# Kernel tuning notes

Hardware: AMD Instinct MI355X
Metric: run time of the kernel (lower is better)

## Reference

```python
import jax, jax.numpy as jnp
import numpy as np

B, S, D = 2, 2048, 1024
H, DH = 16, 64
C = 64          # chunk_size (sliding window)
WF = 4          # widening factor
FMIN = jnp.finfo(jnp.float32).min


def _ln(x, scale, offset, eps=1e-5):
    mu = jnp.mean(x, axis=-1, keepdims=True)
    var = jnp.var(x, axis=-1, keepdims=True)
    return (x - mu) * jax.lax.rsqrt(var + eps) * scale + offset


def setup_inputs() -> dict:
    key = jax.random.key(0)
    ks = jax.random.split(key, 12)
    std = 0.02
    inp = {
        'x': jax.random.normal(ks[0], (B, S, D), dtype=jnp.float32),
        'causal_mask': jnp.tril(jnp.ones((S, S), dtype=bool))[None, None],  # (1,1,S,S)
        'pos': jax.random.normal(ks[1], (C, D), dtype=jnp.float32),          # pos_0..pos_{C-1}
        'rpe': std * jax.random.normal(ks[2], (H, C), dtype=jnp.float32),
        'Wq': std * jax.random.normal(ks[3], (D, H * DH), dtype=jnp.float32),
        'Wk': std * jax.random.normal(ks[4], (D, H * DH), dtype=jnp.float32),
        'Wv': std * jax.random.normal(ks[5], (D, H * DH), dtype=jnp.float32),
        'Wo': std * jax.random.normal(ks[6], (H * DH, D), dtype=jnp.float32),
        'ln1_scale': jnp.ones((D,), jnp.float32),
        'ln1_offset': jnp.zeros((D,), jnp.float32),
        'W1': std * jax.random.normal(ks[7], (D, WF * D), dtype=jnp.float32),
        'b1': jnp.zeros((WF * D,), jnp.float32),
        'W2': std * jax.random.normal(ks[8], (WF * D, D), dtype=jnp.float32),
        'b2': jnp.zeros((D,), jnp.float32),
        'ln2_scale': jnp.ones((D,), jnp.float32),
        'ln2_offset': jnp.zeros((D,), jnp.float32),
    }
    return inp


def _sliding_window_mask(rpe, seq_len):
    # mask[h,t,T] = rpe[h, t-T] if 0 <= t-T < C (lower diagonals), else -inf
    d = jnp.arange(seq_len)[:, None] - jnp.arange(seq_len)[None, :]  # (S,S)
    valid = (d >= 0) & (d < C)
    dc = jnp.clip(d, 0, C - 1)
    val = jnp.where(valid[None], rpe[:, dc], 0.0)  # (H,S,S)
    return jnp.where(val != 0, val, FMIN)


def reference(x, causal_mask, pos, rpe, Wq, Wk, Wv, Wo, ln1_scale, ln1_offset,
              W1, b1, W2, b2, ln2_scale, ln2_offset):
    seq_len = x.shape[1]
    # front/rear positional vectors: pos_i added at positions i, i+C, i+2C, ...
    h = x + pos[jnp.arange(seq_len) % C]  # (B,S,D)

    q = (h @ Wq).reshape(B, seq_len, H, DH)
    k = (h @ Wk).reshape(B, seq_len, H, DH)
    v = (h @ Wv).reshape(B, seq_len, H, DH)

    attn = jnp.einsum('bthd,bThd->bhtT', q, k) * (1.0 / jnp.sqrt(DH))
    attn = attn + _sliding_window_mask(rpe, seq_len)[None]  # learned diag bias
    attn = jnp.where(causal_mask, attn, FMIN)
    attn = jax.nn.softmax(attn, axis=-1)

    out = jnp.einsum('bhtT,bThd->bthd', attn, v).reshape(B, seq_len, H * DH)
    out = out @ Wo

    # dropout_prob = 0 -> identity
    attention = _ln(h + out, ln1_scale, ln1_offset)
    ff = jax.nn.relu(attention @ W1 + b1) @ W2 + b2
    return _ln(ff + attention, ln2_scale, ln2_offset)
```

## Files before the change

### kernel.cpp

```cpp
#include <hip/hip_runtime.h>
#include <hip/hip_bf16.h>

#define DEVI static __device__ __forceinline__

typedef __attribute__((ext_vector_type(4))) float f32x4;
typedef __attribute__((ext_vector_type(8))) short bf16x8;
typedef __attribute__((ext_vector_type(4))) short s16x4;

constexpr int TB  = 2;
constexpr int TS  = 2048;
constexpr int TD  = 1024;
constexpr int TH  = 16;
constexpr int TDH = 64;
constexpr int TC  = 64;
constexpr int TFF = 4096;
constexpr int TM  = TB * TS;

DEVI float bf2f(short s) {
  return __builtin_bit_cast(float, (unsigned)((unsigned short)s) << 16);
}
DEVI short f2bf(float f) {
  return __builtin_bit_cast(short, __float2bfloat16(f));
}

#define GLD16(gp, lp)                                              \
  __builtin_amdgcn_global_load_lds(                                \
      (const __attribute__((address_space(1))) void*)(gp),         \
      (__attribute__((address_space(3))) void*)(lp), 16, 0, 0)

#define WAITVM(N) asm volatile("s_waitcnt vmcnt(" #N ")" ::: "memory")

__global__ __launch_bounds__(256) void k_transpose_bf16(
    const float* __restrict__ W, __hip_bfloat16* __restrict__ WT, int K, int N) {
  __shared__ float tile[32][33];
  int n0 = blockIdx.x * 32, k0 = blockIdx.y * 32;
  int tx = threadIdx.x & 31, ty = threadIdx.x >> 5;
  for (int i = 0; i < 32; i += 8)
    tile[ty + i][tx] = W[(size_t)(k0 + ty + i) * N + n0 + tx];
  __syncthreads();
  for (int i = 0; i < 32; i += 8)
    WT[(size_t)(n0 + ty + i) * K + k0 + tx] = __float2bfloat16(tile[tx][ty + i]);
}

__global__ __launch_bounds__(256) void k_addpos(
    const float* __restrict__ x, const float* __restrict__ pos,
    __hip_bfloat16* __restrict__ hb, int total4) {
  int i = blockIdx.x * 256 + threadIdx.x;
  if (i >= total4) return;
  int e = i * 4;
  int d = e & (TD - 1);
  int t = (e / TD) & (TS - 1);
  f32x4 xv = *(const f32x4*)(x + e);
  f32x4 pv = *(const f32x4*)(pos + (size_t)(t & (TC - 1)) * TD + d);
  s16x4 hb4;
  for (int j = 0; j < 4; j++) hb4[j] = f2bf(xv[j] + pv[j]);
  *(s16x4*)((short*)hb + e) = hb4;
}

template <int EPI>
__global__ __launch_bounds__(256, 3) void k_gemm(
    const __hip_bfloat16* __restrict__ A, const __hip_bfloat16* __restrict__ BT,
    void* __restrict__ Cout, const float* __restrict__ bias,
    int M, int N, int K, int lda, int ldb) {
  constexpr int BM = 128, BN = 128, BK = 32;
  __shared__ __align__(16) __hip_bfloat16 As[3][BM * BK];
  __shared__ __align__(16) __hip_bfloat16 Bs[3][BN * BK];
  int tid = threadIdx.x;
  int lane = tid & 63, wave = tid >> 6;
  int wm = wave >> 1, wn = wave & 1;
  int fr = lane & 15, fg = lane >> 4;
  int m0 = blockIdx.x * BM, n0 = blockIdx.y * BN;
  size_t koff = (size_t)blockIdx.z * K;
  const __hip_bfloat16* Ab = A + koff;
  const __hip_bfloat16* Bb = BT + koff;

  auto stage = [&](int s, int k0) {
#pragma unroll
    for (int i = 0; i < 2; i++) {
      int c = (wave * 2 + i) * 64 + lane;
      int row = c >> 2, seg = (c & 3) ^ ((row >> 1) & 3);
      GLD16(Ab + (size_t)(m0 + row) * lda + k0 + seg * 8,
            (char*)&As[s][0] + (wave * 2 + i) * 1024);
      GLD16(Bb + (size_t)(n0 + row) * ldb + k0 + seg * 8,
            (char*)&Bs[s][0] + (wave * 2 + i) * 1024);
    }
  };

  f32x4 acc[4][4] = {};
  const int nt = K / BK;
  stage(0, 0);
  stage(1, BK);
  int cur = 0;
  for (int t = 0; t < nt; t++) {
    if (t + 1 < nt) { WAITVM(4); } else { WAITVM(0); }
    __builtin_amdgcn_s_barrier();
    asm volatile("" ::: "memory");
    bf16x8 af[4], bfv[4];
#pragma unroll
    for (int m = 0; m < 4; m++) {
      int row = wm * 64 + m * 16 + fr;
      af[m] = *(const bf16x8*)((const char*)&As[cur][0] + row * 64 +
                               ((fg ^ ((row >> 1) & 3)) * 16));
    }
#pragma unroll
    for (int n = 0; n < 4; n++) {
      int row = wn * 64 + n * 16 + fr;
      bfv[n] = *(const bf16x8*)((const char*)&Bs[cur][0] + row * 64 +
                                ((fg ^ ((row >> 1) & 3)) * 16));
    }
    if (t + 2 < nt) {
      int nb = cur + 2; if (nb >= 3) nb -= 3;
      stage(nb, (t + 2) * BK);
    }
    __builtin_amdgcn_s_setprio(1);
#pragma unroll
    for (int m = 0; m < 4; m++)
#pragma unroll
      for (int n = 0; n < 4; n++)
        acc[m][n] = __builtin_amdgcn_mfma_f32_16x16x32_bf16(af[m], bfv[n],
                                                            acc[m][n], 0, 0, 0);
    __builtin_amdgcn_s_setprio(0);
    cur++; if (cur == 3) cur = 0;
  }

  float* Cf = (float*)Cout + (size_t)blockIdx.z * M * N;
#pragma unroll
  for (int m = 0; m < 4; m++)
#pragma unroll
    for (int n = 0; n < 4; n++) {
      int col = n0 + wn * 64 + n * 16 + fr;
#pragma unroll
      for (int j = 0; j < 4; j++) {
        int row = m0 + wm * 64 + m * 16 + fg * 4 + j;
        float v = acc[m][n][j];
        if (EPI == 1) { v += bias[col]; v = fmaxf(v, 0.f); }
        if (EPI == 2)
          Cf[(size_t)row * N + col] = v;
        else
          ((__hip_bfloat16*)Cout)[(size_t)row * N + col] = __float2bfloat16(v);
      }
    }
}

__global__ __launch_bounds__(256) void k_vtrans(
    const __hip_bfloat16* __restrict__ qkv, __hip_bfloat16* __restrict__ vT) {
  __shared__ short tile[64][68];
  int bh = blockIdx.x;
  int tb = blockIdx.y;
  int b = bh >> 4, h = bh & 15;
  int tid = threadIdx.x;
#pragma unroll
  for (int i = 0; i < 2; i++) {
    int c = i * 256 + tid;
    int trow = c >> 3, seg = c & 7;
    bf16x8 v = *(const bf16x8*)((const short*)qkv +
        (size_t)(b * TS + tb * 64 + trow) * 3072 + 2048 + h * TDH + seg * 8);
    s16x4 lo = {v[0], v[1], v[2], v[3]}, hi = {v[4], v[5], v[6], v[7]};
    *(s16x4*)&tile[trow][seg * 8] = lo;
    *(s16x4*)&tile[trow][seg * 8 + 4] = hi;
  }
  __syncthreads();
#pragma unroll
  for (int i2 = 0; i2 < 2; i2++) {
    int c = i2 * 256 + tid;
    int d = c >> 3, ts = c & 7;
    bf16x8 o;
#pragma unroll
    for (int j = 0; j < 8; j++) o[j] = tile[ts * 8 + j][d];
    *(bf16x8*)((short*)vT + (size_t)bh * TDH * TS + (size_t)d * TS +
               tb * 64 + ts * 8) = o;
  }
}

__global__ __launch_bounds__(256) void k_attn(
    const __hip_bfloat16* __restrict__ qkv, const __hip_bfloat16* __restrict__ vT,
    const float* __restrict__ rpe, __hip_bfloat16* __restrict__ out) {
  __shared__ __align__(16) short K_lds[128 * 64];
  __shared__ __align__(16) short VT_lds[64 * 128];
  __shared__ __align__(16) short P_lds[4][16 * 136];
  __shared__ float rpe_lds[TC];
  int tid = threadIdx.x, lane = tid & 63, wave = tid >> 6;
  int fr = lane & 15, g = lane >> 4;
  int blk = blockIdx.x;
  int qt = blk & 31, bh = blk >> 5;
  int h = bh & 15, b = bh >> 4;
  int t0 = qt * 64;
  const short* qg = (const short*)qkv;

  if (tid < TC) rpe_lds[tid] = rpe[h * TC + tid];

#pragma unroll
  for (int i = 0; i < 4; i++) {
    int cb = i * 256 + wave * 64;
    int c = cb + lane;
    int row = c >> 3, slot = c & 7;
    int seg = slot ^ (row & 7);
    int kr = t0 - 64 + row; if (kr < 0) kr = 0;
    GLD16(qg + ((size_t)(b * TS + kr) * 3072 + 1024 + h * TDH + seg * 8),
          (char*)K_lds + cb * 16);
  }
  const short* vg = (const short*)vT + (size_t)bh * TDH * TS;
#pragma unroll
  for (int i = 0; i < 4; i++) {
    int cb = i * 256 + wave * 64;
    int c = cb + lane;
    int row = c >> 4, slot = c & 15;
    int seg = slot ^ (row & 15);
    int tc = t0 - 64 + seg * 8; if (tc < 0) tc = 0;
    GLD16(vg + (size_t)row * TS + tc, (char*)VT_lds + cb * 16);
  }

  int qrow = t0 + wave * 16 + fr;
  const short* qptr = qg + ((size_t)(b * TS + qrow) * 3072 + h * TDH + g * 8);
  bf16x8 qf0 = *(const bf16x8*)qptr;
  bf16x8 qf1 = *(const bf16x8*)(qptr + 32);

  __syncthreads();

  f32x4 S[8] = {};
#pragma unroll
  for (int kk = 0; kk < 2; kk++) {
    bf16x8 a = kk ? qf1 : qf0;
#pragma unroll
    for (int nt = 0; nt < 8; nt++) {
      int row = nt * 16 + fr;
      int slot = (kk * 4 + g) ^ (row & 7);
      bf16x8 bfrag = *(const bf16x8*)((const char*)K_lds + row * 128 + slot * 16);
      S[nt] = __builtin_amdgcn_mfma_f32_16x16x32_bf16(a, bfrag, S[nt], 0, 0, 0);
    }
  }

  int wq = wave * 16;
#pragma unroll
  for (int r = 0; r < 4; r++) {
    int ql = g * 4 + r;
    float sc[8];
    float m = -3.4028235e38f;
#pragma unroll
    for (int nt = 0; nt < 8; nt++) {
      int jj = nt * 16 + fr;
      int d = wq + ql + 64 - jj;
      bool valid = (d >= 0) && (d < TC) && (t0 - 64 + jj >= 0);
      float v = valid ? (S[nt][r] * 0.125f + rpe_lds[d & (TC - 1)])
                      : -3.4028235e38f;
      sc[nt] = v;
      m = fmaxf(m, v);
    }
#pragma unroll
    for (int o = 1; o < 16; o <<= 1) m = fmaxf(m, __shfl_xor(m, o));
    float p[8], sum = 0.f;
#pragma unroll
    for (int nt = 0; nt < 8; nt++) { p[nt] = __expf(sc[nt] - m); sum += p[nt]; }
#pragma unroll
    for (int o = 1; o < 16; o <<= 1) sum += __shfl_xor(sum, o);
    float rs = 1.0f / sum;
#pragma unroll
    for (int nt = 0; nt < 8; nt++)
      P_lds[wave][ql * 136 + nt * 16 + fr] = f2bf(p[nt] * rs);
  }

  f32x4 O[4] = {};
#pragma unroll
  for (int kk = 0; kk < 4; kk++) {
    bf16x8 pa = *(const bf16x8*)((const char*)&P_lds[wave][0] +
                                 fr * 272 + kk * 64 + g * 16);
#pragma unroll
    for (int dt = 0; dt < 4; dt++) {
      int row = dt * 16 + fr;
      int slot = (kk * 4 + g) ^ (row & 15);
      bf16x8 vb = *(const bf16x8*)((const char*)VT_lds + row * 256 + slot * 16);
      O[dt] = __builtin_amdgcn_mfma_f32_16x16x32_bf16(pa, vb, O[dt], 0, 0, 0);
    }
  }

  size_t ob = ((size_t)(b * TS + t0 + wq + g * 4)) * TD + h * TDH;
#pragma unroll
  for (int dt = 0; dt < 4; dt++)
#pragma unroll
    for (int r = 0; r < 4; r++)
      ((short*)out)[ob + (size_t)r * TD + dt * 16 + fr] = f2bf(O[dt][r]);
}

DEVI float block_sum(float v, float* red) {
  for (int o = 32; o; o >>= 1) v += __shfl_xor(v, o);
  int wave = threadIdx.x >> 6;
  if ((threadIdx.x & 63) == 0) red[wave] = v;
  __syncthreads();
  float r = red[0] + red[1] + red[2] + red[3];
  __syncthreads();
  return r;
}

__global__ __launch_bounds__(256) void k_ln1(
    const float* __restrict__ x, const float* __restrict__ pos,
    const float* __restrict__ P0, const float* __restrict__ P1,
    const float* __restrict__ scale, const float* __restrict__ offset,
    float* __restrict__ outf, __hip_bfloat16* __restrict__ outb) {
  __shared__ float red[4];
  int row = blockIdx.x, tid = threadIdx.x;
  int t = row & (TS - 1), pr = t & (TC - 1);
  size_t base = (size_t)row * TD + tid * 4;
  f32x4 xv = *(const f32x4*)(x + base);
  f32x4 pv = *(const f32x4*)(pos + (size_t)pr * TD + tid * 4);
  f32x4 a0 = *(const f32x4*)(P0 + base);
  f32x4 a1 = *(const f32x4*)(P1 + base);
  xv = xv + pv + a0 + a1;
  float s = xv[0] + xv[1] + xv[2] + xv[3];
  s = block_sum(s, red);
  float mu = s * (1.f / TD);
  float s2 = 0.f;
  for (int j = 0; j < 4; j++) { float dlt = xv[j] - mu; s2 += dlt * dlt; }
  s2 = block_sum(s2, red);
  float rs = rsqrtf(s2 * (1.f / TD) + 1e-5f);
  f32x4 sc = *(const f32x4*)(scale + tid * 4);
  f32x4 of = *(const f32x4*)(offset + tid * 4);
  f32x4 y;
  for (int j = 0; j < 4; j++) y[j] = (xv[j] - mu) * rs * sc[j] + of[j];
  *(f32x4*)(outf + base) = y;
  s16x4 pb;
  for (int j = 0; j < 4; j++) pb[j] = f2bf(y[j]);
  *(s16x4*)((short*)outb + base) = pb;
}

__global__ __launch_bounds__(256) void k_ln2(
    const float* __restrict__ P0, const float* __restrict__ P1,
    const float* __restrict__ R, const float* __restrict__ bias,
    const float* __restrict__ scale, const float* __restrict__ offset,
    float* __restrict__ outf) {
  __shared__ float red[4];
  int row = blockIdx.x, tid = threadIdx.x;
  size_t base = (size_t)row * TD + tid * 4;
  f32x4 a0 = *(const f32x4*)(P0 + base);
  f32x4 a1 = *(const f32x4*)(P1 + base);
  f32x4 rv = *(const f32x4*)(R + base);
  f32x4 bi = *(const f32x4*)(bias + tid * 4);
  f32x4 xv = a0 + a1 + rv + bi;
  float s = xv[0] + xv[1] + xv[2] + xv[3];
  s = block_sum(s, red);
  float mu = s * (1.f / TD);
  float s2 = 0.f;
  for (int j = 0; j < 4; j++) { float dlt = xv[j] - mu; s2 += dlt * dlt; }
  s2 = block_sum(s2, red);
  float rs = rsqrtf(s2 * (1.f / TD) + 1e-5f);
  f32x4 sc = *(const f32x4*)(scale + tid * 4);
  f32x4 of = *(const f32x4*)(offset + tid * 4);
  f32x4 y;
  for (int j = 0; j < 4; j++) y[j] = (xv[j] - mu) * rs * sc[j] + of[j];
  *(f32x4*)(outf + base) = y;
}

extern "C" void kernel_launch(void* const* d_in, const int* in_sizes, int n_in,
                              void* d_out, int out_size, void* d_ws, size_t ws_size,
                              hipStream_t stream) {
  const float* x    = (const float*)d_in[0];
  const float* pos  = (const float*)d_in[2];
  const float* rpe  = (const float*)d_in[3];
  const float* Wq   = (const float*)d_in[4];
  const float* Wk   = (const float*)d_in[5];
  const float* Wv   = (const float*)d_in[6];
  const float* Wo   = (const float*)d_in[7];
  const float* ln1s = (const float*)d_in[8];
  const float* ln1o = (const float*)d_in[9];
  const float* W1   = (const float*)d_in[10];
  const float* b1   = (const float*)d_in[11];
  const float* W2   = (const float*)d_in[12];
  const float* b2   = (const float*)d_in[13];
  const float* ln2s = (const float*)d_in[14];
  const float* ln2o = (const float*)d_in[15];

  char* ws = (char*)d_ws;
  const size_t MB = 1ull << 20;
  __hip_bfloat16* WqkvT = (__hip_bfloat16*)(ws + 0 * MB);
  __hip_bfloat16* WoT   = (__hip_bfloat16*)(ws + 6 * MB);
  __hip_bfloat16* W1T   = (__hip_bfloat16*)(ws + 8 * MB);
  __hip_bfloat16* W2T   = (__hip_bfloat16*)(ws + 16 * MB);
  __hip_bfloat16* hB    = (__hip_bfloat16*)(ws + 24 * MB);
  __hip_bfloat16* qkv   = (__hip_bfloat16*)(ws + 32 * MB);
  __hip_bfloat16* aoB   = (__hip_bfloat16*)(ws + 56 * MB);
  float*          oF2   = (float*)(ws + 64 * MB);
  float*          atF   = (float*)(ws + 96 * MB);
  __hip_bfloat16* atB   = (__hip_bfloat16*)(ws + 24 * MB);
  __hip_bfloat16* ff1   = (__hip_bfloat16*)(ws + 32 * MB);
  float*          ff2   = (float*)(ws + 64 * MB);
  __hip_bfloat16* vTb   = (__hip_bfloat16*)(ws + 112 * MB);

  dim3 blk(256);

  k_transpose_bf16<<<dim3(TD / 32, TD / 32), blk, 0, stream>>>(Wq, WqkvT, TD, TD);
  k_transpose_bf16<<<dim3(TD / 32, TD / 32), blk, 0, stream>>>(Wk, WqkvT + (size_t)TD * TD, TD, TD);
  k_transpose_bf16<<<dim3(TD / 32, TD / 32), blk, 0, stream>>>(Wv, WqkvT + (size_t)2 * TD * TD, TD, TD);
  k_transpose_bf16<<<dim3(TD / 32, TD / 32), blk, 0, stream>>>(Wo, WoT, TD, TD);
  k_transpose_bf16<<<dim3(TFF / 32, TD / 32), blk, 0, stream>>>(W1, W1T, TD, TFF);
  k_transpose_bf16<<<dim3(TD / 32, TFF / 32), blk, 0, stream>>>(W2, W2T, TFF, TD);

  k_addpos<<<(TM * TD / 4 + 255) / 256, blk, 0, stream>>>(x, pos, hB, TM * TD / 4);

  k_gemm<0><<<dim3(TM / 128, 3072 / 128, 1), blk, 0, stream>>>(
      hB, WqkvT, qkv, nullptr, TM, 3072, TD, TD, TD);

  k_vtrans<<<dim3(TB * TH, TS / 64), blk, 0, stream>>>(qkv, vTb);
  k_attn<<<TB * TH * (TS / 64), blk, 0, stream>>>(qkv, vTb, rpe, aoB);

  k_gemm<2><<<dim3(TM / 128, TD / 128, 2), blk, 0, stream>>>(
      aoB, WoT, oF2, nullptr, TM, TD, TD / 2, TD, TD);

  k_ln1<<<TM, blk, 0, stream>>>(x, pos, oF2, oF2 + (size_t)TM * TD, ln1s, ln1o, atF, atB);

  k_gemm<1><<<dim3(TM / 128, TFF / 128, 1), blk, 0, stream>>>(
      atB, W1T, ff1, b1, TM, TFF, TD, TD, TD);

  k_gemm<2><<<dim3(TM / 128, TD / 128, 2), blk, 0, stream>>>(
      ff1, W2T, ff2, nullptr, TM, TD, TFF / 2, TFF, TFF);

  k_ln2<<<TM, blk, 0, stream>>>(ff2, ff2 + (size_t)TM * TD, atF, b2, ln2s, ln2o,
                                (float*)d_out);
}
```

Measured before the change: 217.0 us.

## Enlarge GEMM tiles to 256xBN with 8 waves and 4-stage pipeline

Replaces the 128x128 GEMM kernel with a 512-thread, 8-wave kernel using 256-row tiles and 256- or 128-column tiles. It adds a fourth LDS buffer for a deeper prefetch pipeline and splits the A and B staging around two MFMA halves. The larger tiles raise data reuse per block and cut global traffic, but use more registers and LDS. The smaller grids (e.g. 16x12 for QKV) may underfill the 256 CUs.

```diff
diff --git a/kernel.cpp b/kernel.cpp
--- a/kernel.cpp
+++ b/kernel.cpp
@@ -57,83 +57,120 @@
   *(s16x4*)((short*)hb + e) = hb4;
 }
 
-template <int EPI>
-__global__ __launch_bounds__(256, 3) void k_gemm(
+template <int BN, int EPI>
+__global__ __launch_bounds__(512, 2) void k_gemm2(
     const __hip_bfloat16* __restrict__ A, const __hip_bfloat16* __restrict__ BT,
     void* __restrict__ Cout, const float* __restrict__ bias,
     int M, int N, int K, int lda, int ldb) {
-  constexpr int BM = 128, BN = 128, BK = 32;
-  __shared__ __align__(16) __hip_bfloat16 As[3][BM * BK];
-  __shared__ __align__(16) __hip_bfloat16 Bs[3][BN * BK];
+  constexpr int BM = 256, BK = 32;
+  constexpr int FN = BN / 64;
+  constexpr int LPB = BN / 128;
+  __shared__ __align__(16) short As[4][BM * BK];
+  __shared__ __align__(16) short Bs[4][BN * BK];
   int tid = threadIdx.x;
   int lane = tid & 63, wave = tid >> 6;
-  int wm = wave >> 1, wn = wave & 1;
+  int wm = wave >> 2, wn = wave & 3;
   int fr = lane & 15, fg = lane >> 4;
   int m0 = blockIdx.x * BM, n0 = blockIdx.y * BN;
   size_t koff = (size_t)blockIdx.z * K;
   const __hip_bfloat16* Ab = A + koff;
   const __hip_bfloat16* Bb = BT + koff;
 
-  auto stage = [&](int s, int k0) {
+  auto stageA = [&](int d, int T) {
 #pragma unroll
     for (int i = 0; i < 2; i++) {
-      int c = (wave * 2 + i) * 64 + lane;
+      int c = i * 512 + tid;
       int row = c >> 2, seg = (c & 3) ^ ((row >> 1) & 3);
-      GLD16(Ab + (size_t)(m0 + row) * lda + k0 + seg * 8,
-            (char*)&As[s][0] + (wave * 2 + i) * 1024);
-      GLD16(Bb + (size_t)(n0 + row) * ldb + k0 + seg * 8,
-            (char*)&Bs[s][0] + (wave * 2 + i) * 1024);
+      GLD16(Ab + (size_t)(m0 + row) * lda + T * BK + seg * 8,
+            (char*)&As[d][0] + (i * 512 + wave * 64) * 16);
     }
   };
-
-  f32x4 acc[4][4] = {};
+  auto stageB = [&](int d, int T) {
+#pragma unroll
+    for (int i = 0; i < LPB; i++) {
+      int c = i * 512 + tid;
+      int row = c >> 2, seg = (c & 3) ^ ((row >> 1) & 3);
+      GLD16(Bb + (size_t)(n0 + row) * ldb + T * BK + seg * 8,
+            (char*)&Bs[d][0] + (i * 512 + wave * 64) * 16);
+    }
+  };
+
+  f32x4 acc[8][FN];
+#pragma unroll
+  for (int m = 0; m < 8; m++)
+#pragma unroll
+    for (int n = 0; n < FN; n++) acc[m][n] = f32x4{0.f, 0.f, 0.f, 0.f};
+
   const int nt = K / BK;
-  stage(0, 0);
-  stage(1, BK);
-  int cur = 0;
+  stageA(0, 0); stageB(0, 0);
+  stageA(1, 1); stageB(1, 1);
+  stageA(2, 2); stageB(2, 2);
+
   for (int t = 0; t < nt; t++) {
-    if (t + 1 < nt) { WAITVM(4); } else { WAITVM(0); }
+    int d = t & 3;
+    if (t < nt - 2) {
+      if (BN == 256) { WAITVM(8); } else { WAITVM(6); }
+    } else if (t == nt - 2) {
+      if (BN == 256) { WAITVM(4); } else { WAITVM(3); }
+    } else {
+      WAITVM(0);
+    }
     __builtin_amdgcn_s_barrier();
     asm volatile("" ::: "memory");
-    bf16x8 af[4], bfv[4];
+
+    bf16x8 a0[4], bf[FN];
 #pragma unroll
     for (int m = 0; m < 4; m++) {
-      int row = wm * 64 + m * 16 + fr;
-      af[m] = *(const bf16x8*)((const char*)&As[cur][0] + row * 64 +
-                               ((fg ^ ((row >> 1) & 3)) * 16));
-    }
-#pragma unroll
-    for (int n = 0; n < 4; n++) {
-      int row = wn * 64 + n * 16 + fr;
-      bfv[n] = *(const bf16x8*)((const char*)&Bs[cur][0] + row * 64 +
-                                ((fg ^ ((row >> 1) & 3)) * 16));
-    }
-    if (t + 2 < nt) {
-      int nb = cur + 2; if (nb >= 3) nb -= 3;
-      stage(nb, (t + 2) * BK);
-    }
+      int row = wm * 128 + m * 16 + fr;
+      a0[m] = *(const bf16x8*)((const char*)&As[d][0] + row * 64 +
+                               ((fg ^ ((row >> 1) & 3)) << 4));
+    }
+#pragma unroll
+    for (int n = 0; n < FN; n++) {
+      int row = wn * (BN / 4) + n * 16 + fr;
+      bf[n] = *(const bf16x8*)((const char*)&Bs[d][0] + row * 64 +
+                               ((fg ^ ((row >> 1) & 3)) << 4));
+    }
+    if (t + 3 < nt) stageA((t + 3) & 3, t + 3);
     __builtin_amdgcn_s_setprio(1);
 #pragma unroll
     for (int m = 0; m < 4; m++)
 #pragma unroll
-      for (int n = 0; n < 4; n++)
-        acc[m][n] = __builtin_amdgcn_mfma_f32_16x16x32_bf16(af[m], bfv[n],
+      for (int n = 0; n < FN; n++)
+        acc[m][n] = __builtin_amdgcn_mfma_f32_16x16x32_bf16(a0[m], bf[n],
                                                             acc[m][n], 0, 0, 0);
     __builtin_amdgcn_s_setprio(0);
-    cur++; if (cur == 3) cur = 0;
+
+    bf16x8 a1[4];
+#pragma unroll
+    for (int m = 0; m < 4; m++) {
+      int row = wm * 128 + 64 + m * 16 + fr;
+      a1[m] = *(const bf16x8*)((const char*)&As[d][0] + row * 64 +
+                               ((fg ^ ((row >> 1) & 3)) << 4));
+    }
+    if (t + 3 < nt) stageB((t + 3) & 3, t + 3);
+    __builtin_amdgcn_s_setprio(1);
+#pragma unroll
+    for (int m = 0; m < 4; m++)
+#pragma unroll
+      for (int n = 0; n < FN; n++)
+        acc[m + 4][n] = __builtin_amdgcn_mfma_f32_16x16x32_bf16(a1[m], bf[n],
+                                                                acc[m + 4][n], 0, 0, 0);
+    __builtin_amdgcn_s_setprio(0);
   }
 
   float* Cf = (float*)Cout + (size_t)blockIdx.z * M * N;
 #pragma unroll
-  for (int m = 0; m < 4; m++)
-#pragma unroll
-    for (int n = 0; n < 4; n++) {
-      int col = n0 + wn * 64 + n * 16 + fr;
+  for (int m = 0; m < 8; m++)
+#pragma unroll
+    for (int n = 0; n < FN; n++) {
+      int col = n0 + wn * (BN / 4) + n * 16 + fr;
+      float bv = (EPI == 1) ? bias[col] : 0.f;
 #pragma unroll
       for (int j = 0; j < 4; j++) {
-        int row = m0 + wm * 64 + m * 16 + fg * 4 + j;
+        int row = m0 + wm * 128 + m * 16 + fg * 4 + j;
         float v = acc[m][n][j];
-        if (EPI == 1) { v += bias[col]; v = fmaxf(v, 0.f); }
+        if (EPI == 1) { v += bv; v = fmaxf(v, 0.f); }
         if (EPI == 2)
           Cf[(size_t)row * N + col] = v;
         else
@@ -384,7 +421,7 @@
   float*          ff2   = (float*)(ws + 64 * MB);
   __hip_bfloat16* vTb   = (__hip_bfloat16*)(ws + 112 * MB);
 
-  dim3 blk(256);
+  dim3 blk(256), blk5(512);
 
   k_transpose_bf16<<<dim3(TD / 32, TD / 32), blk, 0, stream>>>(Wq, WqkvT, TD, TD);
   k_transpose_bf16<<<dim3(TD / 32, TD / 32), blk, 0, stream>>>(Wk, WqkvT + (size_t)TD * TD, TD, TD);
@@ -395,21 +432,21 @@
 
   k_addpos<<<(TM * TD / 4 + 255) / 256, blk, 0, stream>>>(x, pos, hB, TM * TD / 4);
 
-  k_gemm<0><<<dim3(TM / 128, 3072 / 128, 1), blk, 0, stream>>>(
+  k_gemm2<256, 0><<<dim3(TM / 256, 3072 / 256, 1), blk5, 0, stream>>>(
       hB, WqkvT, qkv, nullptr, TM, 3072, TD, TD, TD);
 
   k_vtrans<<<dim3(TB * TH, TS / 64), blk, 0, stream>>>(qkv, vTb);
   k_attn<<<TB * TH * (TS / 64), blk, 0, stream>>>(qkv, vTb, rpe, aoB);
 
-  k_gemm<2><<<dim3(TM / 128, TD / 128, 2), blk, 0, stream>>>(
+  k_gemm2<128, 2><<<dim3(TM / 256, TD / 128, 2), blk5, 0, stream>>>(
       aoB, WoT, oF2, nullptr, TM, TD, TD / 2, TD, TD);
 
   k_ln1<<<TM, blk, 0, stream>>>(x, pos, oF2, oF2 + (size_t)TM * TD, ln1s, ln1o, atF, atB);
 
-  k_gemm<1><<<dim3(TM / 128, TFF / 128, 1), blk, 0, stream>>>(
+  k_gemm2<256, 1><<<dim3(TM / 256, TFF / 256, 1), blk5, 0, stream>>>(
       atB, W1T, ff1, b1, TM, TFF, TD, TD, TD);
 
-  k_gemm<2><<<dim3(TM / 128, TD / 128, 2), blk, 0, stream>>>(
+  k_gemm2<128, 2><<<dim3(TM / 256, TD / 128, 2), blk5, 0, stream>>>(
       ff1, W2T, ff2, nullptr, TM, TD, TFF / 2, TFF, TFF);
 
   k_ln2<<<TM, blk, 0, stream>>>(ff2, ff2 + (size_t)TM * TD, atF, b2, ln2s, ln2o,
```

After: 213.9 us. About the same (-1.4%).
